# Kernel tuning notes

Measured on AMD Instinct MI355X. Metric: run time of the kernel, lower is better.

Reference implementation:

```python
import jax, jax.numpy as jnp
import numpy as np
from jax import lax

DIM, HEADS, POOL = 512, 8, 16
HD = DIM // HEADS
SCALE = HD ** -0.5


def _cbs(x, w, s, b, d=1, g=1):
    """Conv2d(bias=False, pad=d*(k-1)//2) + folded BN (scale,bias) + SiLU."""
    k = w.shape[-1]
    p = d * (k - 1) // 2
    y = lax.conv_general_dilated(x, w, (1, 1), [(p, p), (p, p)],
                                 rhs_dilation=(d, d), feature_group_count=g,
                                 dimension_numbers=("NCHW", "OIHW", "NCHW"))
    y = y * s[None, :, None, None] + b[None, :, None, None]
    return y * jax.nn.sigmoid(y)  # SiLU


def _forward(x, w01, s01, b01, w02, s02, b02, w03, s03, b03,
             w12, s12, b12, w13, s13, b13, w22, s22, b22, w23, s23, b23,
             w3, s3, b3, wkv, skv, bkv, wfc1, bfc1, wfc2, bfc2):
    bsz, c, h, w = x.shape
    # ---- _MutilScal ----
    a01 = _cbs(x, w01, s01, b01)                       # [b,128,h,w]
    a03 = _cbs(_cbs(a01, w02, s02, b02, d=3, g=128), w03, s03, b03)
    a13 = _cbs(_cbs(a01, w12, s12, b12, d=5, g=128), w13, s13, b13)
    a23 = _cbs(_cbs(a01, w22, s22, b22, d=7, g=128), w23, s23, b23)
    attn = _cbs(a03 + a13 + a23, w3, s3, b3) * x       # [b,512,h,w]
    # AdaptiveAvgPool2d(POOL): exact block mean since h,w divisible by POOL
    pooled = attn.reshape(bsz, c, POOL, h // POOL, POOL, w // POOL).mean(axis=(3, 5))
    kv = _cbs(pooled, wkv, skv, bkv)                   # [b,1024,16,16]
    # ---- pooled cross-attention ----
    n, n1 = h * w, POOL * POOL
    q = x.reshape(bsz, HEADS, HD, n).transpose(0, 1, 3, 2)          # [b,H,n,d]
    kvr = kv.reshape(bsz, 2, HEADS, HD, n1)
    k = kvr[:, 0].transpose(0, 1, 3, 2)                              # [b,H,n1,d]
    v = kvr[:, 1].transpose(0, 1, 3, 2)                              # [b,H,n1,d]
    dots = jnp.einsum("bhnd,bhmd->bhnm", q, k) * SCALE
    a = jax.nn.softmax(dots, axis=-1)
    o = jnp.einsum("bhnm,bhmd->bhnd", a, v)                          # [b,H,n,d]
    attn_out = o.transpose(0, 1, 3, 2).reshape(bsz, c, h, w)
    # ---- SE channel gate ----
    gap = x.mean(axis=(2, 3))                                        # [b,c]
    y = jnp.clip(gap @ wfc1[:, :, 0, 0].T + bfc1, 0.0, 6.0)          # ReLU6
    gate = jax.nn.sigmoid(y @ wfc2[:, :, 0, 0].T + bfc2)             # [b,c]
    c_attn = gate[:, :, None, None] * x
    return attn_out + c_attn


def setup_inputs() -> dict:
    key = jax.random.key(0)
    ks = jax.random.split(key, 32)
    ki = iter(ks)
    f = jnp.float32

    def rn(shape, scale=0.05):
        return (jax.random.normal(next(ki), shape, dtype=f) * scale)

    inp = {"x": jax.random.normal(next(ki), (8, DIM, 64, 64), dtype=f)}
    inp.update(w01=rn((128, 512, 1, 1)), s01=jnp.ones((128,), f), b01=rn((128,)))
    inp.update(w02=rn((128, 1, 3, 3)), s02=jnp.ones((128,), f), b02=rn((128,)))
    inp.update(w03=rn((512, 128, 1, 1)), s03=jnp.ones((512,), f), b03=rn((512,)))
    inp.update(w12=rn((128, 1, 3, 3)), s12=jnp.ones((128,), f), b12=rn((128,)))
    inp.update(w13=rn((512, 128, 1, 1)), s13=jnp.ones((512,), f), b13=rn((512,)))
    inp.update(w22=rn((128, 1, 3, 3)), s22=jnp.ones((128,), f), b22=rn((128,)))
    inp.update(w23=rn((512, 128, 1, 1)), s23=jnp.ones((512,), f), b23=rn((512,)))
    inp.update(w3=rn((512, 512, 1, 1)), s3=jnp.ones((512,), f), b3=rn((512,)))
    inp.update(wkv=rn((1024, 512, 1, 1)), skv=jnp.ones((1024,), f), bkv=rn((1024,)))
    inp.update(wfc1=rn((128, 512, 1, 1)), bfc1=rn((128,)))
    inp.update(wfc2=rn((512, 128, 1, 1)), bfc2=rn((512,)))
    return inp


def reference(x, w01, s01, b01, w02, s02, b02, w03, s03, b03,
              w12, s12, b12, w13, s13, b13, w22, s22, b22, w23, s23, b23,
              w3, s3, b3, wkv, skv, bkv, wfc1, bfc1, wfc2, bfc2):
    return _forward(x, w01, s01, b01, w02, s02, b02, w03, s03, b03,
                    w12, s12, b12, w13, s13, b13, w22, s22, b22, w23, s23, b23,
                    w3, s3, b3, wkv, skv, bkv, wfc1, bfc1, wfc2, bfc2)
```

## Files before the change

### kernel.cpp

```cpp
#include <hip/hip_runtime.h>
#include <cstddef>


static __device__ __forceinline__ float silu_f(float v) {
  return v / (1.f + __expf(-v));
}

typedef __attribute__((ext_vector_type(8))) short short8v;
typedef __attribute__((ext_vector_type(4))) float f32x4;

union FragU { unsigned u[4]; short8v v; uint4 q; };

#define VM_WAIT(N) asm volatile("s_waitcnt vmcnt(" #N ")" ::: "memory")
#define SBAR()     asm volatile("s_barrier" ::: "memory")

static __device__ __forceinline__ unsigned short f2bf(float f) {
  unsigned u = __builtin_bit_cast(unsigned, f);
  u += 0x7fffu + ((u >> 16) & 1u);
  return (unsigned short)(u >> 16);
}
static __device__ __forceinline__ unsigned packbf(float lo, float hi) {
  return (unsigned)f2bf(lo) | ((unsigned)f2bf(hi) << 16);
}
static __device__ __forceinline__ float bf_lo(unsigned w) {
  return __builtin_bit_cast(float, w << 16);
}
static __device__ __forceinline__ float bf_hi(unsigned w) {
  return __builtin_bit_cast(float, w & 0xffff0000u);
}

static __device__ __forceinline__ void gload16(const unsigned* gsrc, unsigned* ldst) {
  __builtin_amdgcn_global_load_lds(
      (const __attribute__((address_space(1))) unsigned*)gsrc,
      (__attribute__((address_space(3))) unsigned*)ldst, 16, 0, 0);
}

static __device__ __forceinline__ void stage_tile_g(const unsigned* __restrict__ src,
                                                    unsigned* dst, int tid) {
  gload16(src + 4 * tid, dst + 4 * tid);
  gload16(src + 4 * (tid + 512), dst + 4 * (tid + 512));
}

static __device__ __forceinline__ short8v load_frag4(const unsigned* P, int ksg, int pos) {
  FragU f;
  f.q = *(const uint4*)(P + (((ksg << 7) + pos) << 2));
  return f.v;
}

static __device__ __forceinline__ void xload16(const float* __restrict__ src, int ld,
                                               int tid, float v[16]) {
  const int pos = tid & 127, kg = tid >> 7;
  const float* p = src + pos + (size_t)(kg * 16) * ld;
#pragma unroll
  for (int i = 0; i < 16; ++i) v[i] = p[(size_t)i * ld];
}
static __device__ __forceinline__ void xload16_sum2(const float* __restrict__ a,
                                                    const float* __restrict__ b2, int ld,
                                                    int tid, float v[16]) {
  const int pos = tid & 127, kg = tid >> 7;
  const float* pA = a + pos + (size_t)(kg * 16) * ld;
  const float* pB = b2 + pos + (size_t)(kg * 16) * ld;
#pragma unroll
  for (int i = 0; i < 16; ++i) v[i] = pA[(size_t)i * ld] + pB[(size_t)i * ld];
}
static __device__ __forceinline__ void xwrite16(const float v[16], unsigned* Xp, int tid) {
  const int pos = tid & 127, kg = tid >> 7;
#pragma unroll
  for (int i2 = 0; i2 < 4; ++i2) {
    const int kq = kg * 4 + i2;
    const int r4 = (kq & 3) + ((kq >> 3) << 2);
    const int sub = (kq >> 2) & 1;
    uint2 wv;
    wv.x = packbf(v[i2 * 4 + 0], v[i2 * 4 + 1]);
    wv.y = packbf(v[i2 * 4 + 2], v[i2 * 4 + 3]);
    *(uint2*)(Xp + (((r4 << 7) + pos) << 2) + sub * 2) = wv;
  }
}

static __device__ __forceinline__ void stage_x_pack(const float* __restrict__ src, int ld,
                                                    unsigned* Xp, int tid) {
  float v[16];
  xload16(src, ld, tid, v);
  xwrite16(v, Xp, tid);
}

#define GEMM_IDS                                            \
  const int tid = threadIdx.x;                              \
  const int w = tid >> 6, lane = tid & 63;                  \
  const int g = lane >> 4, nl = lane & 15;                  \
  const int wr = w >> 1, wc = w & 1;

#define GEMM_KSTEP_B(ACC, XB, WB)                                                  \
  _Pragma("unroll")                                                                \
  for (int ks = 0; ks < 2; ++ks) {                                                 \
    const short8v a0 = load_frag4(WB, ks * 4 + g, wr * 32 + nl);                   \
    const short8v a1 = load_frag4(WB, ks * 4 + g, wr * 32 + 16 + nl);              \
    _Pragma("unroll")                                                              \
    for (int jj = 0; jj < 4; ++jj) {                                               \
      const short8v bfr = load_frag4(XB, ks * 4 + g, wc * 64 + jj * 16 + nl);      \
      ACC[0][jj] = __builtin_amdgcn_mfma_f32_16x16x32_bf16(a0, bfr, ACC[0][jj], 0, 0, 0); \
      ACC[1][jj] = __builtin_amdgcn_mfma_f32_16x16x32_bf16(a1, bfr, ACC[1][jj], 0, 0, 0); \
    }                                                                              \
  }

__global__ __launch_bounds__(256)
void prepack_w_kernel(const float* __restrict__ w01, const float* __restrict__ w03,
                      const float* __restrict__ w13, const float* __restrict__ w23,
                      const float* __restrict__ w3, const float* __restrict__ wkv,
                      unsigned* __restrict__ img)
{
  const int t = blockIdx.x;
  const float* W; int K; int tile; unsigned* base;
  if (t < 8)       { W = w01; K = 512; tile = t;      base = img; }
  else if (t < 16) { W = w03; K = 128; tile = t - 8;  base = img + 32768; }
  else if (t < 24) { W = w13; K = 128; tile = t - 16; base = img + 65536; }
  else if (t < 32) { W = w23; K = 128; tile = t - 24; base = img + 98304; }
  else if (t < 64) { W = w3;  K = 512; tile = t - 32; base = img + 131072; }
  else             { W = wkv; K = 512; tile = t - 64; base = img + 262144; }
  const int nk = K >> 6;
  const int to = tile / nk, tk = tile - to * nk;
  unsigned* dst = base + (size_t)tile * 4096;
  for (int wi = threadIdx.x; wi < 4096; wi += 256) {
    const int r4 = wi >> 9, pos = (wi >> 2) & 127, sub = (wi >> 1) & 1, j = wi & 1;
    const int kq = (r4 & 3) + sub * 4 + ((r4 >> 2) << 3);
    const int k = tk * 64 + 4 * kq + 2 * j;
    const int oc = to * 128 + pos;
    dst[wi] = packbf(W[(size_t)oc * K + k], W[(size_t)oc * K + k + 1]);
  }
}

__global__ __launch_bounds__(512)
void gemm_a01_kernel(const float* __restrict__ X, const unsigned* __restrict__ Wimg,
                     const float* __restrict__ sc, const float* __restrict__ bi,
                     unsigned* __restrict__ A01p)
{
  const int b = blockIdx.z, p0 = blockIdx.x * 128;
  GEMM_IDS
  __shared__ unsigned Xp[2][4096], Wp[2][4096];
  const float* Xbase = X + (size_t)b * 512 * 4096 + p0;

  f32x4 acc[2][4];
#pragma unroll
  for (int i = 0; i < 2; ++i)
#pragma unroll
    for (int jj = 0; jj < 4; ++jj) acc[i][jj] = (f32x4){0.f, 0.f, 0.f, 0.f};

  {
    float vx[16];
    xload16(Xbase, 4096, tid, vx);
    stage_tile_g(Wimg, Wp[0], tid);
    xwrite16(vx, Xp[0], tid);
  }
  __syncthreads();

  for (int st = 0; st < 8; ++st) {
    const int cur = st & 1;
    float vn[16];
    if (st < 7) {
      xload16(Xbase + (size_t)((st + 1) * 64) * 4096, 4096, tid, vn);
      stage_tile_g(Wimg + (size_t)(st + 1) * 4096, Wp[cur ^ 1], tid);
    }
    GEMM_KSTEP_B(acc, Xp[cur], Wp[cur])
    if (st < 7) xwrite16(vn, Xp[cur ^ 1], tid);
    __syncthreads();
  }

#pragma unroll
  for (int i = 0; i < 2; ++i) {
    const int base = wr * 32 + i * 16 + 4 * g;
    const float s0_ = sc[base + 0], b0_ = bi[base + 0];
    const float s1_ = sc[base + 1], b1_ = bi[base + 1];
    const float s2_ = sc[base + 2], b2_ = bi[base + 2];
    const float s3_ = sc[base + 3], b3_ = bi[base + 3];
#pragma unroll
    for (int jj = 0; jj < 4; ++jj) {
      const int pos = p0 + wc * 64 + jj * 16 + nl;
      const float v0 = silu_f(s0_ * acc[i][jj][0] + b0_);
      const float v1 = silu_f(s1_ * acc[i][jj][1] + b1_);
      const float v2 = silu_f(s2_ * acc[i][jj][2] + b2_);
      const float v3 = silu_f(s3_ * acc[i][jj][3] + b3_);
      A01p[((size_t)b * 64 + (base >> 1)) * 4096 + pos]     = packbf(v0, v1);
      A01p[((size_t)b * 64 + (base >> 1) + 1) * 4096 + pos] = packbf(v2, v3);
    }
  }
}

__global__ __launch_bounds__(256)
void dwconv_pack_kernel(const unsigned* __restrict__ A01p, unsigned* __restrict__ Timg,
                        const float* __restrict__ w02, const float* __restrict__ s02, const float* __restrict__ b02,
                        const float* __restrict__ w12, const float* __restrict__ s12, const float* __restrict__ b12,
                        const float* __restrict__ w22, const float* __restrict__ s22, const float* __restrict__ b22)
{
  const int br = blockIdx.z;
  const int yb = blockIdx.y;
  const int b = yb >> 4, t16 = yb & 15, kstep = t16 >> 3, mm = t16 & 7;
  const int kq = (mm & 3) + ((mm >> 2) << 3);
  const int cbase = kstep * 64 + kq * 4;
  const int p = blockIdx.x * 256 + threadIdx.x;
  const int y = p >> 6, xx = p & 63;
  const int d = 3 + 2 * br;

  const float* wsel = br == 0 ? w02 : (br == 1 ? w12 : w22);
  const float* ssel = br == 0 ? s02 : (br == 1 ? s12 : s22);
  const float* bsel = br == 0 ? b02 : (br == 1 ? b12 : b22);

  float sum[8] = {};
  const unsigned* plane0 = A01p + ((size_t)b * 64 + (cbase >> 1)) * 4096;

#pragma unroll
  for (int u = -1; u <= 1; ++u) {
    const int yv = y + u * d;
    if ((unsigned)yv < 64u) {
#pragma unroll
      for (int v = -1; v <= 1; ++v) {
        const int xv = xx + v * d;
        if ((unsigned)xv < 64u) {
          const int idx = yv * 64 + xv;
          const int tap = (u + 1) * 3 + (v + 1);
#pragma unroll
          for (int q = 0; q < 4; ++q) {
            const int sub = q >> 1, jw = q & 1;
            const unsigned wv = plane0[(size_t)(sub * 8 + jw) * 4096 + idx];
            const int ch = cbase + sub * 16 + jw * 2;
            sum[q * 2 + 0] += wsel[(ch + 0) * 9 + tap] * bf_lo(wv);
            sum[q * 2 + 1] += wsel[(ch + 1) * 9 + tap] * bf_hi(wv);
          }
        }
      }
    }
  }

  unsigned wout[4];
#pragma unroll
  for (int h = 0; h < 4; ++h) {
    const int ch = cbase + (h >> 1) * 16 + (h & 1) * 2;
    const float va = silu_f(ssel[ch] * sum[h * 2] + bsel[ch]);
    const float vb = silu_f(ssel[ch + 1] * sum[h * 2 + 1] + bsel[ch + 1]);
    wout[h] = packbf(va, vb);
  }
  const int tile = ((br * 8 + b) * 2 + kstep) * 32 + (p >> 7);
  *(uint4*)(Timg + (size_t)tile * 4096 + (((mm << 7) + (p & 127)) << 2)) = *(uint4*)wout;
}

__global__ __launch_bounds__(512)
void gemm3branch_img_kernel(const unsigned* __restrict__ Timg, const unsigned* __restrict__ Wimg3,
                            const float* __restrict__ s0, const float* __restrict__ s1, const float* __restrict__ s2,
                            const float* __restrict__ b0, const float* __restrict__ b1, const float* __restrict__ b2,
                            unsigned* __restrict__ Bimg)
{
  const int b = blockIdx.z, pt = blockIdx.x, oc0 = blockIdx.y * 128;
  GEMM_IDS
  __shared__ unsigned Xp[2][4096], Wp[2][4096];

  float sum[2][4][4] = {};
  f32x4 acc[2][4];
#pragma unroll
  for (int i = 0; i < 2; ++i)
#pragma unroll
    for (int jj = 0; jj < 4; ++jj) acc[i][jj] = (f32x4){0.f, 0.f, 0.f, 0.f};

#define SRC_X3(st) (Timg + (((size_t)(((st) >> 1) * 8 + b) * 2 + ((st) & 1)) * 32 + pt) * 4096)
#define SRC_W3(st) (Wimg3 + (size_t)((st) >> 1) * 32768 + ((size_t)(oc0 >> 7) * 2 + ((st) & 1)) * 4096)

  stage_tile_g(SRC_X3(0), Xp[0], tid);
  stage_tile_g(SRC_W3(0), Wp[0], tid);
  __syncthreads();

  for (int st = 0; st < 6; ++st) {
    const int cur = st & 1;
    if (st < 5) {
      stage_tile_g(SRC_X3(st + 1), Xp[cur ^ 1], tid);
      stage_tile_g(SRC_W3(st + 1), Wp[cur ^ 1], tid);
    }
    GEMM_KSTEP_B(acc, Xp[cur], Wp[cur])
    if (st & 1) {
      const int brn = st >> 1;
      const float* ss = brn == 0 ? s0 : (brn == 1 ? s1 : s2);
      const float* bs = brn == 0 ? b0 : (brn == 1 ? b1 : b2);
#pragma unroll
      for (int i = 0; i < 2; ++i) {
        const int base = oc0 + wr * 32 + i * 16 + 4 * g;
#pragma unroll
        for (int r = 0; r < 4; ++r) {
          const float s = ss[base + r], bb = bs[base + r];
#pragma unroll
          for (int jj = 0; jj < 4; ++jj) {
            sum[i][jj][r] += silu_f(s * acc[i][jj][r] + bb);
            acc[i][jj][r] = 0.f;
          }
        }
      }
    }
    __syncthreads();
  }
#undef SRC_X3
#undef SRC_W3

#pragma unroll
  for (int i = 0; i < 2; ++i) {
    const int ol = wr * 32 + i * 16 + 4 * g;
    const int kstep_g = (oc0 + ol) >> 6;
    const int kin = ol & 63;
    const int kq2 = kin >> 2;
    const int r4 = (kq2 & 3) + ((kq2 >> 3) << 2);
    const int sub = (kq2 >> 2) & 1;
#pragma unroll
    for (int jj = 0; jj < 4; ++jj) {
      const int pos = wc * 64 + jj * 16 + nl;
      uint2 wv;
      wv.x = packbf(sum[i][jj][0], sum[i][jj][1]);
      wv.y = packbf(sum[i][jj][2], sum[i][jj][3]);
      *(uint2*)(Bimg + ((size_t)(b * 8 + kstep_g) * 32 + pt) * 4096 + (((r4 << 7) + pos) << 2) + sub * 2) = wv;
    }
  }
}

__global__ __launch_bounds__(512)
void gemm_pool_img_kernel(const unsigned* __restrict__ Bimg, const unsigned* __restrict__ W3img,
                          const float* __restrict__ sc, const float* __restrict__ bi,
                          const float* __restrict__ xin, float* __restrict__ pooled2,
                          float* __restrict__ gapb)
{
  const int b = blockIdx.z, pt = blockIdx.x, oc0 = blockIdx.y * 128;
  const int p0 = pt * 128;
  const float* xb = xin + (size_t)b * 512 * 4096;
  GEMM_IDS
  __shared__ unsigned Xp[2][4096], Wp[2][4096];

  f32x4 acc[2][4];
#pragma unroll
  for (int i = 0; i < 2; ++i)
#pragma unroll
    for (int jj = 0; jj < 4; ++jj) acc[i][jj] = (f32x4){0.f, 0.f, 0.f, 0.f};

#define SRC_XP(st) (Bimg + ((size_t)(b * 8 + (st)) * 32 + pt) * 4096)
#define SRC_WP(st) (W3img + ((size_t)(oc0 >> 7) * 8 + (st)) * 4096)

  stage_tile_g(SRC_XP(0), Xp[0], tid);
  stage_tile_g(SRC_WP(0), Wp[0], tid);
  stage_tile_g(SRC_XP(1), Xp[1], tid);
  stage_tile_g(SRC_WP(1), Wp[1], tid);

#pragma unroll
  for (int st = 0; st < 8; ++st) {
    const int cur = st & 1;
    if (st < 7) { VM_WAIT(4); } else { VM_WAIT(0); }
    SBAR();
    GEMM_KSTEP_B(acc, Xp[cur], Wp[cur])
    SBAR();
    if (st < 6) {
      stage_tile_g(SRC_XP(st + 2), Xp[cur], tid);
      stage_tile_g(SRC_WP(st + 2), Wp[cur], tid);
    }
  }
#undef SRC_XP
#undef SRC_WP

  float* red  = (float*)Wp[0];
  float* gred = red + 2048;
  for (int e = tid; e < 2176; e += 512) red[e] = 0.f;
  __syncthreads();

  float xsum[2][4] = {};
#pragma unroll
  for (int i = 0; i < 2; ++i)
#pragma unroll
    for (int r = 0; r < 4; ++r) {
      const int ol = wr * 32 + i * 16 + 4 * g + r;
      const int oc = oc0 + ol;
      const float s = sc[oc], bb = bi[oc];
#pragma unroll
      for (int jj = 0; jj < 4; ++jj) {
        const int p = p0 + wc * 64 + jj * 16 + nl;
        const float xv = xb[(size_t)oc * 4096 + p];
        xsum[i][r] += xv;
        float val = silu_f(s * acc[i][jj][r] + bb) * xv;
        val += __shfl_xor(val, 1, 64);
        val += __shfl_xor(val, 2, 64);
        if ((nl & 3) == 0) {
          const int col = p & 63;
          atomicAdd(&red[ol * 16 + (col >> 2)], val);
        }
      }
    }
#pragma unroll
  for (int i = 0; i < 2; ++i)
#pragma unroll
    for (int r = 0; r < 4; ++r) {
      float v = xsum[i][r];
      v += __shfl_xor(v, 1, 64);
      v += __shfl_xor(v, 2, 64);
      v += __shfl_xor(v, 4, 64);
      v += __shfl_xor(v, 8, 64);
      if (nl == 0)
        atomicAdd(&gred[wr * 32 + i * 16 + 4 * g + r], v);
    }
  __syncthreads();

  {
    const int ph = pt >> 1;
    float* pdst = pooled2 + (size_t)(pt & 1) * (8ull * 512 * 256);
    for (int e = tid; e < 2048; e += 512) {
      const int ol = e >> 4, pw = e & 15;
      pdst[((size_t)b * 512 + oc0 + ol) * 256 + ph * 16 + pw] = red[e] * (1.f / 16.f);
    }
    if (tid < 128)
      atomicAdd(&gapb[b * 512 + oc0 + tid], gred[tid]);
  }
}

__global__ __launch_bounds__(512)
void gemm_kv_kernel(const float* __restrict__ pooled2, const unsigned* __restrict__ WKVimg,
                    const float* __restrict__ sc, const float* __restrict__ bi,
                    unsigned* __restrict__ Kimg, unsigned* __restrict__ Vimg)
{
  const int b = blockIdx.z, p0 = blockIdx.x * 128, oc0 = blockIdx.y * 128;
  const float* XbA = pooled2 + (size_t)b * 512 * 256 + p0;
  const float* XbB = XbA + 8ull * 512 * 256;
  GEMM_IDS
  __shared__ unsigned Xp[2][4096], Wp[2][4096];

  f32x4 acc[2][4];
#pragma unroll
  for (int i = 0; i < 2; ++i)
#pragma unroll
    for (int jj = 0; jj < 4; ++jj) acc[i][jj] = (f32x4){0.f, 0.f, 0.f, 0.f};

  {
    float vx[16];
    xload16_sum2(XbA, XbB, 256, tid, vx);
    stage_tile_g(WKVimg + (size_t)(oc0 >> 7) * 8 * 4096, Wp[0], tid);
    xwrite16(vx, Xp[0], tid);
  }
  __syncthreads();

  for (int st = 0; st < 8; ++st) {
    const int cur = st & 1;
    float vn[16];
    if (st < 7) {
      xload16_sum2(XbA + (size_t)((st + 1) * 64) * 256, XbB + (size_t)((st + 1) * 64) * 256,
                   256, tid, vn);
      stage_tile_g(WKVimg + ((size_t)(oc0 >> 7) * 8 + st + 1) * 4096, Wp[cur ^ 1], tid);
    }
    GEMM_KSTEP_B(acc, Xp[cur], Wp[cur])
    if (st < 7) xwrite16(vn, Xp[cur ^ 1], tid);
    __syncthreads();
  }

  const bool isK = (oc0 < 512);
#pragma unroll
  for (int i = 0; i < 2; ++i) {
    const int ocb = oc0 + wr * 32 + i * 16 + 4 * g;
#pragma unroll
    for (int jj = 0; jj < 4; ++jj) {
      const int pos = p0 + wc * 64 + jj * 16 + nl;
      float v[4];
#pragma unroll
      for (int r = 0; r < 4; ++r)
        v[r] = silu_f(sc[ocb + r] * acc[i][jj][r] + bi[ocb + r]);
      const int ch = pos >> 7, ml = pos & 127;
      if (isK) {
        const int h = ocb >> 6, d0 = ocb & 63;
        const int kq = d0 >> 2, sub = (kq >> 2) & 1;
        const int r4 = (kq & 3) + ((kq >> 3) << 2);
        unsigned* t = Kimg + ((size_t)(b * 8 + h) * 2 + ch) * 4096;
        uint2 wv;
        wv.x = packbf(v[0] * 0.125f, v[1] * 0.125f);
        wv.y = packbf(v[2] * 0.125f, v[3] * 0.125f);
        *(uint2*)(t + (((r4 << 7) + ml) << 2) + sub * 2) = wv;
      } else {
        const int h = (ocb - 512) >> 6, d0 = (ocb - 512) & 63;
        unsigned* t = Vimg + ((size_t)(b * 8 + h) * 2 + ch) * 4096;
        float ov[4];
#pragma unroll
        for (int r = 0; r < 4; ++r) ov[r] = __shfl_xor(v[r], 1, 64);
        if ((nl & 1) == 0) {
          const int s = (ml >> 1) & 1, m4 = ml >> 2;
#pragma unroll
          for (int r = 0; r < 4; ++r)
            t[((m4 * 64 + d0 + r) << 1) + s] = packbf(v[r], ov[r]);
        }
      }
    }
  }
}

__global__ __launch_bounds__(512)
void se_kernel(const float* __restrict__ gap,
               const float* __restrict__ wfc1, const float* __restrict__ bfc1,
               const float* __restrict__ wfc2, const float* __restrict__ bfc2,
               float* __restrict__ gate)
{
  const int b = blockIdx.x, tid = threadIdx.x;
  __shared__ float ylds[128];
  if (tid < 128) {
    float a = 0.f;
    for (int c = 0; c < 512; ++c) a += gap[b * 512 + c] * wfc1[tid * 512 + c];
    a = a * (1.f / 4096.f) + bfc1[tid];
    ylds[tid] = fminf(fmaxf(a, 0.f), 6.f);
  }
  __syncthreads();
  float g = 0.f;
  for (int j = 0; j < 128; ++j) g += ylds[j] * wfc2[tid * 128 + j];
  g += bfc2[tid];
  gate[b * 512 + tid] = 1.f / (1.f + __expf(-g));
}

__global__ __launch_bounds__(512)
void attn_mfma_kernel(const float* __restrict__ x, const unsigned* __restrict__ Kimg,
                      const unsigned* __restrict__ Vimg,
                      const float* __restrict__ gate, float* __restrict__ out)
{
  const int b = blockIdx.z, h = blockIdx.y;
  const int n0 = blockIdx.x * 128;
  const int tid = threadIdx.x;
  const int w = tid >> 6, lane = tid & 63;
  const int g = lane >> 4, nl = lane & 15;

  __shared__ unsigned lds[20480];
  unsigned* Qp = lds;
  unsigned* Kb0 = lds + 4096;
  unsigned* Kb1 = lds + 8192;
  unsigned* Vb0 = lds + 12288;
  unsigned* Vb1 = lds + 16384;
  float* Osm = (float*)(lds + 4096);

  const size_t tbase = (size_t)(b * 8 + h) * 2 * 4096;

  stage_tile_g(Kimg + tbase, Kb0, tid);
  stage_tile_g(Vimg + tbase, Vb0, tid);
  stage_x_pack(x + ((size_t)b * 512 + h * 64) * 4096 + n0, 4096, Qp, tid);
  __syncthreads();
  stage_tile_g(Kimg + tbase + 4096, Kb1, tid);
  stage_tile_g(Vimg + tbase + 4096, Vb1, tid);

  float m_run = -1e30f, l_run = 0.f;
  f32x4 o[4];
#pragma unroll
  for (int i = 0; i < 4; ++i) o[i] = (f32x4){0.f, 0.f, 0.f, 0.f};

#pragma unroll
  for (int ch = 0; ch < 2; ++ch) {
    const unsigned* Kp = ch ? Kb1 : Kb0;
    const unsigned* Vp = ch ? Vb1 : Vb0;

    f32x4 s[8];
#pragma unroll
    for (int mb = 0; mb < 8; ++mb) s[mb] = (f32x4){0.f, 0.f, 0.f, 0.f};
#pragma unroll
    for (int ks = 0; ks < 2; ++ks) {
      const short8v qf = load_frag4(Qp, ks * 4 + g, w * 16 + nl);
#pragma unroll
      for (int mb = 0; mb < 8; ++mb) {
        const short8v kf = load_frag4(Kp, ks * 4 + g, mb * 16 + nl);
        s[mb] = __builtin_amdgcn_mfma_f32_16x16x32_bf16(kf, qf, s[mb], 0, 0, 0);
      }
    }

    float cm = -1e30f;
#pragma unroll
    for (int mb = 0; mb < 8; ++mb)
#pragma unroll
      for (int r = 0; r < 4; ++r) cm = fmaxf(cm, s[mb][r]);
    cm = fmaxf(cm, __shfl_xor(cm, 16, 64));
    cm = fmaxf(cm, __shfl_xor(cm, 32, 64));
    const float mnew = fmaxf(m_run, cm);
    const float corr = __expf(m_run - mnew);
    m_run = mnew;
    float cs = 0.f;
#pragma unroll
    for (int mb = 0; mb < 8; ++mb)
#pragma unroll
      for (int r = 0; r < 4; ++r) {
        const float p = __expf(s[mb][r] - mnew);
        s[mb][r] = p;
        cs += p;
      }
    cs += __shfl_xor(cs, 16, 64);
    cs += __shfl_xor(cs, 32, 64);
    l_run = l_run * corr + cs;
#pragma unroll
    for (int db = 0; db < 4; ++db)
#pragma unroll
      for (int r = 0; r < 4; ++r) o[db][r] *= corr;

#pragma unroll
    for (int ks = 0; ks < 4; ++ks) {
      FragU pf;
      pf.u[0] = packbf(s[2 * ks][0],     s[2 * ks][1]);
      pf.u[1] = packbf(s[2 * ks][2],     s[2 * ks][3]);
      pf.u[2] = packbf(s[2 * ks + 1][0], s[2 * ks + 1][1]);
      pf.u[3] = packbf(s[2 * ks + 1][2], s[2 * ks + 1][3]);
#pragma unroll
      for (int db = 0; db < 4; ++db) {
        FragU vf;
        const uint2 lo = *(const uint2*)(Vp + ((8 * ks + g) * 64 + db * 16 + nl) * 2);
        const uint2 hi = *(const uint2*)(Vp + ((8 * ks + 4 + g) * 64 + db * 16 + nl) * 2);
        vf.u[0] = lo.x; vf.u[1] = lo.y; vf.u[2] = hi.x; vf.u[3] = hi.y;
        o[db] = __builtin_amdgcn_mfma_f32_16x16x32_bf16(vf.v, pf.v, o[db], 0, 0, 0);
      }
    }
    __syncthreads();
  }

  const float inv = 1.f / l_run;
#pragma unroll
  for (int db = 0; db < 4; ++db)
#pragma unroll
    for (int r = 0; r < 4; ++r)
      Osm[(db * 16 + 4 * g + r) * 132 + w * 16 + nl] = o[db][r] * inv;
  __syncthreads();

  {
    const int n = tid & 127, t7 = tid >> 7;
    const int jw = t7 >> 1, half = t7 & 1;
#pragma unroll
    for (int i = 0; i < 16; ++i) {
      const int d = t7 + 4 * i;
      const int r4 = (i & 3) + ((i >> 3) << 2);
      const int sub = (i >> 2) & 1;
      const unsigned xw = Qp[(((r4 << 7) + n) << 2) + sub * 2 + jw];
      const float xv = half ? bf_hi(xw) : bf_lo(xw);
      const int c2 = h * 64 + d;
      const size_t off = ((size_t)b * 512 + c2) * 4096 + n0 + n;
      out[off] = Osm[d * 132 + n] + gate[b * 512 + c2] * xv;
    }
  }
}

extern "C" void kernel_launch(void* const* d_in, const int* in_sizes, int n_in,
                              void* d_out, int out_size, void* d_ws, size_t ws_size,
                              hipStream_t stream)
{
  const float* x    = (const float*)d_in[0];
  const float* w01  = (const float*)d_in[1];
  const float* s01  = (const float*)d_in[2];
  const float* b01  = (const float*)d_in[3];
  const float* w02  = (const float*)d_in[4];
  const float* s02  = (const float*)d_in[5];
  const float* b02  = (const float*)d_in[6];
  const float* w03  = (const float*)d_in[7];
  const float* s03  = (const float*)d_in[8];
  const float* b03  = (const float*)d_in[9];
  const float* w12  = (const float*)d_in[10];
  const float* s12  = (const float*)d_in[11];
  const float* b12  = (const float*)d_in[12];
  const float* w13  = (const float*)d_in[13];
  const float* s13  = (const float*)d_in[14];
  const float* b13  = (const float*)d_in[15];
  const float* w22  = (const float*)d_in[16];
  const float* s22  = (const float*)d_in[17];
  const float* b22  = (const float*)d_in[18];
  const float* w23  = (const float*)d_in[19];
  const float* s23  = (const float*)d_in[20];
  const float* b23  = (const float*)d_in[21];
  const float* w3   = (const float*)d_in[22];
  const float* s3   = (const float*)d_in[23];
  const float* b3   = (const float*)d_in[24];
  const float* wkv  = (const float*)d_in[25];
  const float* skv  = (const float*)d_in[26];
  const float* bkv  = (const float*)d_in[27];
  const float* wfc1 = (const float*)d_in[28];
  const float* bfc1 = (const float*)d_in[29];
  const float* wfc2 = (const float*)d_in[30];
  const float* bfc2 = (const float*)d_in[31];

  float* out = (float*)d_out;
  unsigned* wsu = (unsigned*)d_ws;

  unsigned* Timg    = wsu;
  float*    pooled2 = (float*)(wsu + 6291456);
  unsigned* Kimg    = wsu + 8388608;
  unsigned* Vimg    = wsu + 8912896;
  float*    gapb    = (float*)(wsu + 9437184);
  float*    gateb   = (float*)(wsu + 9441280);
  unsigned* Wimg    = wsu + 9445376;

  unsigned* A01p = (unsigned*)d_out;
  unsigned* Bimg = (unsigned*)d_out;

  prepack_w_kernel<<<128, 256, 0, stream>>>(w01, w03, w13, w23, w3, wkv, Wimg);
  gemm_a01_kernel<<<dim3(32, 1, 8), 512, 0, stream>>>(x, Wimg, s01, b01, A01p);
  dwconv_pack_kernel<<<dim3(16, 128, 3), 256, 0, stream>>>(A01p, Timg,
      w02, s02, b02, w12, s12, b12, w22, s22, b22);
  gemm3branch_img_kernel<<<dim3(32, 4, 8), 512, 0, stream>>>(Timg, Wimg + 32768,
      s03, s13, s23, b03, b13, b23, Bimg);
  hipMemsetAsync(gapb, 0, 4096 * sizeof(float), stream);
  gemm_pool_img_kernel<<<dim3(32, 4, 8), 512, 0, stream>>>(Bimg, Wimg + 131072,
      s3, b3, x, pooled2, gapb);
  gemm_kv_kernel<<<dim3(2, 8, 8), 512, 0, stream>>>(pooled2, Wimg + 262144, skv, bkv, Kimg, Vimg);
  se_kernel<<<8, 512, 0, stream>>>(gapb, wfc1, bfc1, wfc2, bfc2, gateb);
  attn_mfma_kernel<<<dim3(32, 8, 8), 512, 0, stream>>>(x, Kimg, Vimg, gateb, out);
}
```

Baseline: 234.3 us.

## Cache bf16-packed x from first GEMM for pool GEMM epilogue reads

The first 1x1-conv GEMM already loads all of x, so it now also writes a bf16 pair-packed copy of x into spare space in the output buffer. The pooling GEMM epilogue reads that packed copy (two 32-bit words for four channels) instead of re-reading fp32 x, with vectorised scale and bias loads. This halves the bytes of the epilogue's x re-read at the cost of extra global stores in the first kernel and bf16 rounding of x in the attention product and the GAP sum. It also raises wave priority around the MFMA k-step.

```diff
diff --git a/kernel.cpp b/kernel.cpp
--- a/kernel.cpp
+++ b/kernel.cpp
@@ -75,6 +75,14 @@
     wv.y = packbf(v[i2 * 4 + 2], v[i2 * 4 + 3]);
     *(uint2*)(Xp + (((r4 << 7) + pos) << 2) + sub * 2) = wv;
   }
+}
+static __device__ __forceinline__ void xstore_pairs(const float v[16],
+                                                    unsigned* __restrict__ Xg_bst,
+                                                    int p0, int tid) {
+  const int pos = tid & 127, kg = tid >> 7;
+#pragma unroll
+  for (int m = 0; m < 8; ++m)
+    Xg_bst[(size_t)(kg * 8 + m) * 4096 + p0 + pos] = packbf(v[2 * m], v[2 * m + 1]);
 }
 
 static __device__ __forceinline__ void stage_x_pack(const float* __restrict__ src, int ld,
@@ -132,12 +140,13 @@
 __global__ __launch_bounds__(512)
 void gemm_a01_kernel(const float* __restrict__ X, const unsigned* __restrict__ Wimg,
                      const float* __restrict__ sc, const float* __restrict__ bi,
-                     unsigned* __restrict__ A01p)
+                     unsigned* __restrict__ A01p, unsigned* __restrict__ Ximg2)
 {
   const int b = blockIdx.z, p0 = blockIdx.x * 128;
   GEMM_IDS
   __shared__ unsigned Xp[2][4096], Wp[2][4096];
   const float* Xbase = X + (size_t)b * 512 * 4096 + p0;
+  unsigned* Xg_b = Ximg2 + (size_t)b * 256 * 4096;
 
   f32x4 acc[2][4];
 #pragma unroll
@@ -150,6 +159,7 @@
     xload16(Xbase, 4096, tid, vx);
     stage_tile_g(Wimg, Wp[0], tid);
     xwrite16(vx, Xp[0], tid);
+    xstore_pairs(vx, Xg_b, p0, tid);
   }
   __syncthreads();
 
@@ -161,7 +171,10 @@
       stage_tile_g(Wimg + (size_t)(st + 1) * 4096, Wp[cur ^ 1], tid);
     }
     GEMM_KSTEP_B(acc, Xp[cur], Wp[cur])
-    if (st < 7) xwrite16(vn, Xp[cur ^ 1], tid);
+    if (st < 7) {
+      xwrite16(vn, Xp[cur ^ 1], tid);
+      xstore_pairs(vn, Xg_b + (size_t)(32 * (st + 1)) * 4096, p0, tid);
+    }
     __syncthreads();
   }
 
@@ -318,12 +331,12 @@
 __global__ __launch_bounds__(512)
 void gemm_pool_img_kernel(const unsigned* __restrict__ Bimg, const unsigned* __restrict__ W3img,
                           const float* __restrict__ sc, const float* __restrict__ bi,
-                          const float* __restrict__ xin, float* __restrict__ pooled2,
+                          const unsigned* __restrict__ Ximg2, float* __restrict__ pooled2,
                           float* __restrict__ gapb)
 {
   const int b = blockIdx.z, pt = blockIdx.x, oc0 = blockIdx.y * 128;
   const int p0 = pt * 128;
-  const float* xb = xin + (size_t)b * 512 * 4096;
+  const unsigned* Xb2 = Ximg2 + (size_t)b * 256 * 4096;
   GEMM_IDS
   __shared__ unsigned Xp[2][4096], Wp[2][4096];
 
@@ -346,7 +359,9 @@
     const int cur = st & 1;
     if (st < 7) { VM_WAIT(4); } else { VM_WAIT(0); }
     SBAR();
+    __builtin_amdgcn_s_setprio(1);
     GEMM_KSTEP_B(acc, Xp[cur], Wp[cur])
+    __builtin_amdgcn_s_setprio(0);
     SBAR();
     if (st < 6) {
       stage_tile_g(SRC_XP(st + 2), Xp[cur], tid);
@@ -363,26 +378,32 @@
 
   float xsum[2][4] = {};
 #pragma unroll
-  for (int i = 0; i < 2; ++i)
-#pragma unroll
-    for (int r = 0; r < 4; ++r) {
-      const int ol = wr * 32 + i * 16 + 4 * g + r;
-      const int oc = oc0 + ol;
-      const float s = sc[oc], bb = bi[oc];
-#pragma unroll
-      for (int jj = 0; jj < 4; ++jj) {
-        const int p = p0 + wc * 64 + jj * 16 + nl;
-        const float xv = xb[(size_t)oc * 4096 + p];
-        xsum[i][r] += xv;
-        float val = silu_f(s * acc[i][jj][r] + bb) * xv;
+  for (int i = 0; i < 2; ++i) {
+    const int olb = wr * 32 + i * 16 + 4 * g;
+    const int oc_ = oc0 + olb;
+    const float4 s4 = *(const float4*)(sc + oc_);
+    const float4 b4 = *(const float4*)(bi + oc_);
+#pragma unroll
+    for (int jj = 0; jj < 4; ++jj) {
+      const int p = p0 + wc * 64 + jj * 16 + nl;
+      const unsigned xw0 = Xb2[(size_t)(oc_ >> 1) * 4096 + p];
+      const unsigned xw1 = Xb2[(size_t)((oc_ >> 1) + 1) * 4096 + p];
+      const float xv[4] = {bf_lo(xw0), bf_hi(xw0), bf_lo(xw1), bf_hi(xw1)};
+      const float sv[4] = {s4.x, s4.y, s4.z, s4.w};
+      const float bv[4] = {b4.x, b4.y, b4.z, b4.w};
+#pragma unroll
+      for (int r = 0; r < 4; ++r) {
+        xsum[i][r] += xv[r];
+        float val = silu_f(sv[r] * acc[i][jj][r] + bv[r]) * xv[r];
         val += __shfl_xor(val, 1, 64);
         val += __shfl_xor(val, 2, 64);
         if ((nl & 3) == 0) {
           const int col = p & 63;
-          atomicAdd(&red[ol * 16 + (col >> 2)], val);
+          atomicAdd(&red[(olb + r) * 16 + (col >> 2)], val);
         }
       }
     }
+  }
 #pragma unroll
   for (int i = 0; i < 2; ++i)
 #pragma unroll
@@ -676,18 +697,19 @@
   float*    gateb   = (float*)(wsu + 9441280);
   unsigned* Wimg    = wsu + 9445376;
 
-  unsigned* A01p = (unsigned*)d_out;
-  unsigned* Bimg = (unsigned*)d_out;
+  unsigned* A01p  = (unsigned*)d_out;
+  unsigned* Bimg  = (unsigned*)d_out;
+  unsigned* Ximg2 = (unsigned*)d_out + 8388608;
 
   prepack_w_kernel<<<128, 256, 0, stream>>>(w01, w03, w13, w23, w3, wkv, Wimg);
-  gemm_a01_kernel<<<dim3(32, 1, 8), 512, 0, stream>>>(x, Wimg, s01, b01, A01p);
+  gemm_a01_kernel<<<dim3(32, 1, 8), 512, 0, stream>>>(x, Wimg, s01, b01, A01p, Ximg2);
   dwconv_pack_kernel<<<dim3(16, 128, 3), 256, 0, stream>>>(A01p, Timg,
       w02, s02, b02, w12, s12, b12, w22, s22, b22);
   gemm3branch_img_kernel<<<dim3(32, 4, 8), 512, 0, stream>>>(Timg, Wimg + 32768,
       s03, s13, s23, b03, b13, b23, Bimg);
   hipMemsetAsync(gapb, 0, 4096 * sizeof(float), stream);
   gemm_pool_img_kernel<<<dim3(32, 4, 8), 512, 0, stream>>>(Bimg, Wimg + 131072,
-      s3, b3, x, pooled2, gapb);
+      s3, b3, Ximg2, pooled2, gapb);
   gemm_kv_kernel<<<dim3(2, 8, 8), 512, 0, stream>>>(pooled2, Wimg + 262144, skv, bkv, Kimg, Vimg);
   se_kernel<<<8, 512, 0, stream>>>(gapb, wfc1, bfc1, wfc2, bfc2, gateb);
   attn_mfma_kernel<<<dim3(32, 8, 8), 512, 0, stream>>>(x, Kimg, Vimg, gateb, out);
```

Result: no change. 233.2 us (median of 3 runs) (-0.5%).
